# Performance work log

Hardware: AMD Instinct MI355X
Metric: run time of the kernel (lower is better)

Reference implementation:

```python
import jax, jax.numpy as jnp
import numpy as np

J6, J3 = 13, 30          # joints with 6-dim and 3-dim outputs (contiguous groups)
J = J6 + J3              # 43 joints total
D = 512                  # latent_dim
B, T = 16, 196


def setup_inputs() -> dict:
    key = jax.random.key(0)
    ks = jax.random.split(key, 7)
    s = 0.02  # weight init scale
    return {
        "x":   jax.random.normal(ks[0], (B, T, J, D), dtype=jnp.float32),
        "W1":  jax.random.normal(ks[1], (J, D, D), dtype=jnp.float32) * s,
        "b1":  jax.random.normal(ks[2], (J, D), dtype=jnp.float32) * s,
        "W2a": jax.random.normal(ks[3], (J6, D, 6), dtype=jnp.float32) * s,
        "b2a": jax.random.normal(ks[4], (J6, 6), dtype=jnp.float32) * s,
        "W2b": jax.random.normal(ks[5], (J3, D, 3), dtype=jnp.float32) * s,
        "b2b": jax.random.normal(ks[6], (J3, 3), dtype=jnp.float32) * s,
    }


def reference(x, W1, b1, W2a, b2a, W2b, b2b):
    # Per-joint MLP: Linear(D,D) -> GELU -> Linear(D,out_dim_j), concatenated
    # over joints along the last dim (heterogeneous 'dk' mode, vectorized).
    h = jnp.einsum('btjd,jde->btje', x, W1) + b1          # [B,T,J,D]
    h = jax.nn.gelu(h, approximate=False)                  # torch nn.GELU (erf)
    oa = jnp.einsum('btjd,jdo->btjo', h[:, :, :J6], W2a) + b2a  # [B,T,13,6]
    ob = jnp.einsum('btjd,jdo->btjo', h[:, :, J6:], W2b) + b2b  # [B,T,30,3]
    b, t = x.shape[0], x.shape[1]
    # torch.cat(out_list, dim=-1) in joint order == group-wise reshape + concat
    motion = jnp.concatenate([oa.reshape(b, t, -1), ob.reshape(b, t, -1)], axis=-1)
    return motion  # [B, T, 13*6 + 30*3] = [B, T, 168]
```

## Files before the change

### kernel.cpp

```cpp
#include <hip/hip_runtime.h>
#include <hip/hip_bf16.h>

typedef unsigned short ushort_t;
typedef short short8 __attribute__((ext_vector_type(8)));
typedef float f32x4 __attribute__((ext_vector_type(4)));

#define J_TOT 43
#define J6 13
#define D_DIM 512
#define BT 3136
#define OUTW 168

__device__ __forceinline__ unsigned short bf16rne(float f) {
    unsigned u = __builtin_bit_cast(unsigned, f);
    u += 0x7fffu + ((u >> 16) & 1u);
    return (unsigned short)(u >> 16);
}

__device__ __forceinline__ float gelu_f(float v) {
    float t = v * __builtin_fmaf(v * v, 0.0356774081f, 0.7978845608f);
    float e = __builtin_amdgcn_exp2f(t * 2.8853900818f);
    float s = __builtin_amdgcn_rcpf(1.0f + e);
    return __builtin_fmaf(-v, s, v);
}

__device__ __forceinline__ void async_ld16(const void* gsrc, void* ldst) {
    __builtin_amdgcn_global_load_lds(
        (const __attribute__((address_space(1))) unsigned int*)(unsigned long long)(const char*)gsrc,
        (__attribute__((address_space(3))) unsigned int*)ldst,
        16, 0, 0);
}

__global__ void w1_transpose_kernel(const float* __restrict__ W1, ushort_t* __restrict__ W1t) {
    __shared__ ushort_t tile[64][74];
    const int j = blockIdx.z;
    const int t = threadIdx.x;
    const int d0 = blockIdx.x * 64, e0 = blockIdx.y * 64;
    const float* src = W1 + (size_t)j * D_DIM * D_DIM;
    const int el = t & 63, dl = t >> 6;
#pragma unroll
    for (int i = 0; i < 16; i++) {
        int d = dl + i * 4;
        tile[el][d] = bf16rne(src[(size_t)(d0 + d) * D_DIM + e0 + el]);
    }
    __syncthreads();
    ushort_t* dst = W1t + (size_t)j * D_DIM * D_DIM;
#pragma unroll
    for (int i = 0; i < 16; i++) {
        int n = dl + i * 4;
        dst[(size_t)(e0 + n) * D_DIM + d0 + el] = tile[n][el];
    }
}

__global__ void w2_pack_kernel(const float* __restrict__ W2a, const float* __restrict__ b2a,
                               const float* __restrict__ W2b, const float* __restrict__ b2b,
                               ushort_t* __restrict__ W2t, float* __restrict__ b2p) {
    const int j = blockIdx.x;
    const int t = threadIdx.x;
    const int odim = (j < J6) ? 6 : 3;
    const float* w = (j < J6) ? (W2a + (size_t)j * D_DIM * 6) : (W2b + (size_t)(j - J6) * D_DIM * 3);
    for (int idx = t; idx < 16 * D_DIM; idx += 256) {
        int o = idx >> 9, k = idx & 511;
        float v = (o < odim) ? w[(size_t)k * odim + o] : 0.0f;
        W2t[(size_t)j * 16 * D_DIM + idx] = bf16rne(v);
    }
    if (t < 16) {
        const float* bb = (j < J6) ? (b2a + (size_t)j * 6) : (b2b + (size_t)(j - J6) * 3);
        b2p[j * 16 + t] = (t < odim) ? bb[t] : 0.0f;
    }
}

__global__ __launch_bounds__(256, 2)
void MotionDecoder_36309653520632_kernel(const float* __restrict__ x,
                                         const float* __restrict__ b1,
                                         const ushort_t* __restrict__ W1t,
                                         const ushort_t* __restrict__ W2t,
                                         const float* __restrict__ b2p,
                                         float* __restrict__ out) {
    __shared__ unsigned char smem[32768];
    char* as_base = (char*)smem;
    char* bs_base = (char*)smem + 16384;
    char* hs_base = (char*)smem;

    const int j   = blockIdx.y;
    const int m0  = blockIdx.x * 128;
    const int tid = threadIdx.x;
    const int lane = tid & 63;
    const int wid  = tid >> 6;
    const int wrow = (wid >> 1) * 64;
    const int wcol = (wid & 1) * 64;

    const int a_m  = tid >> 1;
    const int a_k0 = (tid & 1) * 32;
    int a_row = m0 + a_m; if (a_row > BT - 1) a_row = BT - 1;
    const float* xrow = x + ((size_t)a_row * J_TOT + j) * D_DIM;

    const ushort_t* w1j = W1t + (size_t)j * D_DIM * D_DIM;
    const ushort_t* w2j = W2t + (size_t)j * 16 * D_DIM;

    f32x4 acc2[4];
#pragma unroll
    for (int r = 0; r < 4; r++) acc2[r] = (f32x4){0.f, 0.f, 0.f, 0.f};

    for (int nt = 0; nt < 4; nt++) {
        const int n0 = nt * 128;
        f32x4 acc[4][4];
#pragma unroll
        for (int a = 0; a < 4; a++)
#pragma unroll
            for (int b = 0; b < 4; b++) acc[a][b] = (f32x4){0.f, 0.f, 0.f, 0.f};

        for (int ks = 0; ks < 8; ks++) {
#pragma unroll
            for (int pass = 0; pass < 4; pass++) {
                int n = pass * 32 + wid * 8 + (lane >> 3);
                int cg = (lane & 7) ^ (n & 7);
                const ushort_t* gsrc = w1j + (size_t)(n0 + n) * D_DIM + ks * 64 + cg * 8;
                char* ldst = bs_base + (pass * 32 + wid * 8) * 128;
                async_ld16(gsrc, ldst);
            }
            const float* ap = xrow + ks * 64 + a_k0;
            float4 f[8];
#pragma unroll
            for (int i = 0; i < 8; i++) f[i] = ((const float4*)ap)[i];
#pragma unroll
            for (int c = 0; c < 4; c++) {
                union { unsigned short s[8]; uint4 v; } pk;
                float4 u0 = f[2 * c], u1 = f[2 * c + 1];
                pk.s[0] = bf16rne(u0.x); pk.s[1] = bf16rne(u0.y);
                pk.s[2] = bf16rne(u0.z); pk.s[3] = bf16rne(u0.w);
                pk.s[4] = bf16rne(u1.x); pk.s[5] = bf16rne(u1.y);
                pk.s[6] = bf16rne(u1.z); pk.s[7] = bf16rne(u1.w);
                int ch = (a_k0 >> 3) + c;
                int sw = ch ^ (a_m & 7);
                *(uint4*)(as_base + a_m * 128 + sw * 16) = pk.v;
            }
            __syncthreads();
#pragma unroll
            for (int kk = 0; kk < 2; kk++) {
                short8 af[4], bfr[4];
                int chv = kk * 4 + (lane >> 4);
#pragma unroll
                for (int rt = 0; rt < 4; rt++) {
                    int m = wrow + rt * 16 + (lane & 15);
                    af[rt] = *(const short8*)(as_base + m * 128 + ((chv ^ (m & 7)) * 16));
                }
#pragma unroll
                for (int ct = 0; ct < 4; ct++) {
                    int n = wcol + ct * 16 + (lane & 15);
                    bfr[ct] = *(const short8*)(bs_base + n * 128 + ((chv ^ (n & 7)) * 16));
                }
#pragma unroll
                for (int rt = 0; rt < 4; rt++)
#pragma unroll
                    for (int ct = 0; ct < 4; ct++)
                        acc[rt][ct] = __builtin_amdgcn_mfma_f32_16x16x32_bf16(
                            af[rt], bfr[ct], acc[rt][ct], 0, 0, 0);
            }
            __syncthreads();
        }

#pragma unroll
        for (int ct = 0; ct < 4; ct++) {
            int ncol = wcol + ct * 16 + (lane & 15);
            float bv = b1[j * D_DIM + n0 + ncol];
            int c2 = ncol >> 3;
            int boff = (ncol & 7) * 2;
#pragma unroll
            for (int rt = 0; rt < 4; rt++) {
                int mb = wrow + rt * 16 + ((lane >> 4) << 2);
#pragma unroll
                for (int r = 0; r < 4; r++) {
                    float g = gelu_f(acc[rt][ct][r] + bv);
                    int m = mb + r;
                    int sw = c2 ^ (m & 15);
                    *(unsigned short*)(hs_base + m * 256 + sw * 16 + boff) = bf16rne(g);
                }
            }
        }
        __syncthreads();

        if (wid < 2) {
            short8 wf[4];
#pragma unroll
            for (int kk2 = 0; kk2 < 4; kk2++) {
                const ushort_t* gsrc = w2j + (size_t)(lane & 15) * D_DIM + n0 + kk2 * 32 + (lane >> 4) * 8;
                wf[kk2] = *(const short8*)gsrc;
            }
#pragma unroll
            for (int rt = 0; rt < 4; rt++) {
                int m = wid * 64 + rt * 16 + (lane & 15);
#pragma unroll
                for (int kk2 = 0; kk2 < 4; kk2++) {
                    int ch = kk2 * 4 + (lane >> 4);
                    short8 a2 = *(const short8*)(hs_base + m * 256 + ((ch ^ (m & 15)) * 16));
                    acc2[rt] = __builtin_amdgcn_mfma_f32_16x16x32_bf16(a2, wf[kk2], acc2[rt], 0, 0, 0);
                }
            }
        }
        __syncthreads();
    }

    if (wid < 2) {
        int o = lane & 15;
        int odim = (j < J6) ? 6 : 3;
        int cb = (j < J6) ? j * 6 : 78 + (j - J6) * 3;
        float bo = b2p[j * 16 + o];
        if (o < odim) {
#pragma unroll
            for (int rt = 0; rt < 4; rt++) {
#pragma unroll
                for (int r = 0; r < 4; r++) {
                    int m = m0 + wid * 64 + rt * 16 + ((lane >> 4) << 2) + r;
                    if (m < BT) out[(size_t)m * OUTW + cb + o] = acc2[rt][r] + bo;
                }
            }
        }
    }
}

extern "C" void kernel_launch(void* const* d_in, const int* in_sizes, int n_in,
                              void* d_out, int out_size, void* d_ws, size_t ws_size,
                              hipStream_t stream) {
    const float* x   = (const float*)d_in[0];
    const float* W1  = (const float*)d_in[1];
    const float* b1  = (const float*)d_in[2];
    const float* W2a = (const float*)d_in[3];
    const float* b2a = (const float*)d_in[4];
    const float* W2b = (const float*)d_in[5];
    const float* b2b = (const float*)d_in[6];
    float* out = (float*)d_out;

    ushort_t* W1t = (ushort_t*)d_ws;
    ushort_t* W2t = W1t + (size_t)J_TOT * D_DIM * D_DIM;
    float*    b2p = (float*)(W2t + (size_t)J_TOT * 16 * D_DIM);

    w1_transpose_kernel<<<dim3(8, 8, J_TOT), 256, 0, stream>>>(W1, W1t);
    w2_pack_kernel<<<J_TOT, 256, 0, stream>>>(W2a, b2a, W2b, b2b, W2t, b2p);
    MotionDecoder_36309653520632_kernel<<<dim3(25, J_TOT), 256, 0, stream>>>(
        x, b1, W1t, W2t, b2p, out);
}
```

Before: 654.2 us.

## Pre-convert x to bf16 and stream A tiles via async LDS loads

Adds a separate pass that converts all of x to bf16 in workspace. When the workspace is large enough, the main kernel then loads A tiles with global_load_lds exactly as it loads W1, instead of doing fp32 register loads, per-tile conversion and LDS stores. It also precomputes the per-pass source and destination pointers and raises the launch-bounds occupancy hint from 2 to 4. The cost is an extra full read of x (about 276 MB) plus a bf16 write and re-read, and the whole path depends on the workspace being big enough.

```diff
diff --git a/kernel.cpp b/kernel.cpp
--- a/kernel.cpp
+++ b/kernel.cpp
@@ -29,6 +29,18 @@
         (const __attribute__((address_space(1))) unsigned int*)(unsigned long long)(const char*)gsrc,
         (__attribute__((address_space(3))) unsigned int*)ldst,
         16, 0, 0);
+}
+
+__global__ void x_convert_kernel(const float* __restrict__ x, ushort_t* __restrict__ xb) {
+    size_t i = ((size_t)blockIdx.x * 256 + threadIdx.x) * 8;
+    float4 f0 = *(const float4*)(x + i);
+    float4 f1 = *(const float4*)(x + i + 4);
+    union { unsigned short s[8]; uint4 v; } pk;
+    pk.s[0] = bf16rne(f0.x); pk.s[1] = bf16rne(f0.y);
+    pk.s[2] = bf16rne(f0.z); pk.s[3] = bf16rne(f0.w);
+    pk.s[4] = bf16rne(f1.x); pk.s[5] = bf16rne(f1.y);
+    pk.s[6] = bf16rne(f1.z); pk.s[7] = bf16rne(f1.w);
+    *(uint4*)(xb + i) = pk.v;
 }
 
 __global__ void w1_transpose_kernel(const float* __restrict__ W1, ushort_t* __restrict__ W1t) {
@@ -70,13 +82,15 @@
     }
 }
 
-__global__ __launch_bounds__(256, 2)
-void MotionDecoder_36309653520632_kernel(const float* __restrict__ x,
-                                         const float* __restrict__ b1,
-                                         const ushort_t* __restrict__ W1t,
-                                         const ushort_t* __restrict__ W2t,
-                                         const float* __restrict__ b2p,
-                                         float* __restrict__ out) {
+template <bool XB>
+__global__ __launch_bounds__(256, 4)
+void md_main(const float* __restrict__ x,
+             const ushort_t* __restrict__ xbf,
+             const float* __restrict__ b1,
+             const ushort_t* __restrict__ W1t,
+             const ushort_t* __restrict__ W2t,
+             const float* __restrict__ b2p,
+             float* __restrict__ out) {
     __shared__ unsigned char smem[32768];
     char* as_base = (char*)smem;
     char* bs_base = (char*)smem + 16384;
@@ -90,13 +104,29 @@
     const int wrow = (wid >> 1) * 64;
     const int wcol = (wid & 1) * 64;
 
+    const ushort_t* w1j = W1t + (size_t)j * D_DIM * D_DIM;
+    const ushort_t* w2j = W2t + (size_t)j * 16 * D_DIM;
+
+    const int sg   = lane >> 3;
+    const int cg   = (lane & 7) ^ (sg & 7);
+    const ushort_t* a_src[4];
+    const ushort_t* b_src[4];
+    char* a_dst[4];
+    char* b_dst[4];
+#pragma unroll
+    for (int pass = 0; pass < 4; pass++) {
+        int rr = pass * 32 + wid * 8 + sg;
+        int arow = m0 + rr; if (arow > BT - 1) arow = BT - 1;
+        a_src[pass] = xbf + ((size_t)arow * J_TOT + j) * D_DIM + cg * 8;
+        b_src[pass] = w1j + (size_t)rr * D_DIM + cg * 8;
+        a_dst[pass] = as_base + (pass * 32 + wid * 8) * 128;
+        b_dst[pass] = bs_base + (pass * 32 + wid * 8) * 128;
+    }
+
     const int a_m  = tid >> 1;
     const int a_k0 = (tid & 1) * 32;
     int a_row = m0 + a_m; if (a_row > BT - 1) a_row = BT - 1;
-    const float* xrow = x + ((size_t)a_row * J_TOT + j) * D_DIM;
-
-    const ushort_t* w1j = W1t + (size_t)j * D_DIM * D_DIM;
-    const ushort_t* w2j = W2t + (size_t)j * 16 * D_DIM;
+    const float* xrow = XB ? nullptr : (x + ((size_t)a_row * J_TOT + j) * D_DIM);
 
     f32x4 acc2[4];
 #pragma unroll
@@ -111,29 +141,32 @@
             for (int b = 0; b < 4; b++) acc[a][b] = (f32x4){0.f, 0.f, 0.f, 0.f};
 
         for (int ks = 0; ks < 8; ks++) {
-#pragma unroll
-            for (int pass = 0; pass < 4; pass++) {
-                int n = pass * 32 + wid * 8 + (lane >> 3);
-                int cg = (lane & 7) ^ (n & 7);
-                const ushort_t* gsrc = w1j + (size_t)(n0 + n) * D_DIM + ks * 64 + cg * 8;
-                char* ldst = bs_base + (pass * 32 + wid * 8) * 128;
-                async_ld16(gsrc, ldst);
-            }
-            const float* ap = xrow + ks * 64 + a_k0;
-            float4 f[8];
-#pragma unroll
-            for (int i = 0; i < 8; i++) f[i] = ((const float4*)ap)[i];
-#pragma unroll
-            for (int c = 0; c < 4; c++) {
-                union { unsigned short s[8]; uint4 v; } pk;
-                float4 u0 = f[2 * c], u1 = f[2 * c + 1];
-                pk.s[0] = bf16rne(u0.x); pk.s[1] = bf16rne(u0.y);
-                pk.s[2] = bf16rne(u0.z); pk.s[3] = bf16rne(u0.w);
-                pk.s[4] = bf16rne(u1.x); pk.s[5] = bf16rne(u1.y);
-                pk.s[6] = bf16rne(u1.z); pk.s[7] = bf16rne(u1.w);
-                int ch = (a_k0 >> 3) + c;
-                int sw = ch ^ (a_m & 7);
-                *(uint4*)(as_base + a_m * 128 + sw * 16) = pk.v;
+            const size_t boff = (size_t)n0 * D_DIM + ks * 64;
+            const size_t aoff = (size_t)ks * 64;
+#pragma unroll
+            for (int pass = 0; pass < 4; pass++)
+                async_ld16(b_src[pass] + boff, b_dst[pass]);
+            if (XB) {
+#pragma unroll
+                for (int pass = 0; pass < 4; pass++)
+                    async_ld16(a_src[pass] + aoff, a_dst[pass]);
+            } else {
+                const float* ap = xrow + ks * 64 + a_k0;
+                float4 f[8];
+#pragma unroll
+                for (int i = 0; i < 8; i++) f[i] = ((const float4*)ap)[i];
+#pragma unroll
+                for (int c = 0; c < 4; c++) {
+                    union { unsigned short s[8]; uint4 v; } pk;
+                    float4 u0 = f[2 * c], u1 = f[2 * c + 1];
+                    pk.s[0] = bf16rne(u0.x); pk.s[1] = bf16rne(u0.y);
+                    pk.s[2] = bf16rne(u0.z); pk.s[3] = bf16rne(u0.w);
+                    pk.s[4] = bf16rne(u1.x); pk.s[5] = bf16rne(u1.y);
+                    pk.s[6] = bf16rne(u1.z); pk.s[7] = bf16rne(u1.w);
+                    int ch = (a_k0 >> 3) + c;
+                    int sw = ch ^ (a_m & 7);
+                    *(uint4*)(as_base + a_m * 128 + sw * 16) = pk.v;
+                }
             }
             __syncthreads();
 #pragma unroll
@@ -165,7 +198,7 @@
             int ncol = wcol + ct * 16 + (lane & 15);
             float bv = b1[j * D_DIM + n0 + ncol];
             int c2 = ncol >> 3;
-            int boff = (ncol & 7) * 2;
+            int boff2 = (ncol & 7) * 2;
 #pragma unroll
             for (int rt = 0; rt < 4; rt++) {
                 int mb = wrow + rt * 16 + ((lane >> 4) << 2);
@@ -174,7 +207,7 @@
                     float g = gelu_f(acc[rt][ct][r] + bv);
                     int m = mb + r;
                     int sw = c2 ^ (m & 15);
-                    *(unsigned short*)(hs_base + m * 256 + sw * 16 + boff) = bf16rne(g);
+                    *(unsigned short*)(hs_base + m * 256 + sw * 16 + boff2) = bf16rne(g);
                 }
             }
         }
@@ -234,9 +267,16 @@
     ushort_t* W1t = (ushort_t*)d_ws;
     ushort_t* W2t = W1t + (size_t)J_TOT * D_DIM * D_DIM;
     float*    b2p = (float*)(W2t + (size_t)J_TOT * 16 * D_DIM);
+    ushort_t* xbf = (ushort_t*)((char*)d_ws + 23251648);
+    const size_t ws_needed = 23251648ull + 138084352ull;
 
     w1_transpose_kernel<<<dim3(8, 8, J_TOT), 256, 0, stream>>>(W1, W1t);
     w2_pack_kernel<<<J_TOT, 256, 0, stream>>>(W2a, b2a, W2b, b2b, W2t, b2p);
-    MotionDecoder_36309653520632_kernel<<<dim3(25, J_TOT), 256, 0, stream>>>(
-        x, b1, W1t, W2t, b2p, out);
-}
+
+    if (ws_size >= ws_needed) {
+        x_convert_kernel<<<33712, 256, 0, stream>>>(x, xbf);
+        md_main<true><<<dim3(25, J_TOT), 256, 0, stream>>>(x, xbf, b1, W1t, W2t, b2p, out);
+    } else {
+        md_main<false><<<dim3(25, J_TOT), 256, 0, stream>>>(x, xbf, b1, W1t, W2t, b2p, out);
+    }
+}
```

Result: slower. 768.0 us (+17.4%).

## Keep full bf16 activation row tile resident in LDS and double-buffer W1

Applied to the files above, without the earlier changes.

Loads and converts the 128x512 activation tile for a joint once into a 128 KB LDS buffer, instead of re-reading and converting x for each of the four output column tiles. W1 tiles are now prefetched into registers two steps ahead and written into alternating LDS buffers, replacing the single-buffer async global-to-LDS loads. This cuts global traffic on x several-fold but uses 160 KB of LDS, which drops occupancy to one block per CU and leaves less latency hiding.

```diff
diff --git a/kernel.cpp b/kernel.cpp
--- a/kernel.cpp
+++ b/kernel.cpp
@@ -22,13 +22,6 @@
     float e = __builtin_amdgcn_exp2f(t * 2.8853900818f);
     float s = __builtin_amdgcn_rcpf(1.0f + e);
     return __builtin_fmaf(-v, s, v);
-}
-
-__device__ __forceinline__ void async_ld16(const void* gsrc, void* ldst) {
-    __builtin_amdgcn_global_load_lds(
-        (const __attribute__((address_space(1))) unsigned int*)(unsigned long long)(const char*)gsrc,
-        (__attribute__((address_space(3))) unsigned int*)ldst,
-        16, 0, 0);
 }
 
 __global__ void w1_transpose_kernel(const float* __restrict__ W1, ushort_t* __restrict__ W1t) {
@@ -70,17 +63,18 @@
     }
 }
 
-__global__ __launch_bounds__(256, 2)
-void MotionDecoder_36309653520632_kernel(const float* __restrict__ x,
-                                         const float* __restrict__ b1,
-                                         const ushort_t* __restrict__ W1t,
-                                         const ushort_t* __restrict__ W2t,
-                                         const float* __restrict__ b2p,
-                                         float* __restrict__ out) {
-    __shared__ unsigned char smem[32768];
-    char* as_base = (char*)smem;
-    char* bs_base = (char*)smem + 16384;
-    char* hs_base = (char*)smem;
+__global__ __launch_bounds__(256, 1)
+void md_main(const float* __restrict__ x,
+             const float* __restrict__ b1,
+             const ushort_t* __restrict__ W1t,
+             const ushort_t* __restrict__ W2t,
+             const float* __restrict__ b2p,
+             float* __restrict__ out) {
+    __shared__ unsigned char smem[163840];
+    char* const As = (char*)smem;
+    char* const B0 = (char*)smem + 131072;
+    char* const B1 = (char*)smem + 147456;
+    char* const Hs = (char*)smem + 131072;
 
     const int j   = blockIdx.y;
     const int m0  = blockIdx.x * 128;
@@ -89,66 +83,95 @@
     const int wid  = tid >> 6;
     const int wrow = (wid >> 1) * 64;
     const int wcol = (wid & 1) * 64;
-
-    const int a_m  = tid >> 1;
-    const int a_k0 = (tid & 1) * 32;
-    int a_row = m0 + a_m; if (a_row > BT - 1) a_row = BT - 1;
-    const float* xrow = x + ((size_t)a_row * J_TOT + j) * D_DIM;
+    const int quad = lane >> 4;
+    const int l16  = lane & 15;
 
     const ushort_t* w1j = W1t + (size_t)j * D_DIM * D_DIM;
     const ushort_t* w2j = W2t + (size_t)j * 16 * D_DIM;
 
-    f32x4 acc2[4];
-#pragma unroll
-    for (int r = 0; r < 4; r++) acc2[r] = (f32x4){0.f, 0.f, 0.f, 0.f};
-
-    for (int nt = 0; nt < 4; nt++) {
-        const int n0 = nt * 128;
-        f32x4 acc[4][4];
-#pragma unroll
-        for (int a = 0; a < 4; a++)
-#pragma unroll
-            for (int b = 0; b < 4; b++) acc[a][b] = (f32x4){0.f, 0.f, 0.f, 0.f};
-
-        for (int ks = 0; ks < 8; ks++) {
-#pragma unroll
-            for (int pass = 0; pass < 4; pass++) {
-                int n = pass * 32 + wid * 8 + (lane >> 3);
-                int cg = (lane & 7) ^ (n & 7);
-                const ushort_t* gsrc = w1j + (size_t)(n0 + n) * D_DIM + ks * 64 + cg * 8;
-                char* ldst = bs_base + (pass * 32 + wid * 8) * 128;
-                async_ld16(gsrc, ldst);
-            }
-            const float* ap = xrow + ks * 64 + a_k0;
+    const int bn  = tid >> 1;
+    const int bc0 = (tid & 1) * 4;
+    const ushort_t* bsrc = w1j + (size_t)bn * D_DIM + bc0 * 8;
+    int bws[4];
+#pragma unroll
+    for (int c = 0; c < 4; c++) bws[c] = bn * 128 + (((bc0 + c) ^ (bn & 7)) * 16);
+
+    uint4 pa[4], pb[4];
+#define ISSUE_B(g, p)                                                             \
+    {                                                                             \
+        const ushort_t* s_ = bsrc + (size_t)((g) >> 3) * 128 * D_DIM + ((g) & 7) * 64; \
+        p[0] = *(const uint4*)(s_);      p[1] = *(const uint4*)(s_ + 8);          \
+        p[2] = *(const uint4*)(s_ + 16); p[3] = *(const uint4*)(s_ + 24);         \
+    }
+#define WRITE_B(dst, p)                                                           \
+    {                                                                             \
+        *(uint4*)((dst) + bws[0]) = p[0]; *(uint4*)((dst) + bws[1]) = p[1];       \
+        *(uint4*)((dst) + bws[2]) = p[2]; *(uint4*)((dst) + bws[3]) = p[3];       \
+    }
+
+    ISSUE_B(0, pa);
+    ISSUE_B(1, pb);
+
+    {
+        const int ar = tid >> 1;
+        const int ap = tid & 1;
+        int arow = m0 + ar; if (arow > BT - 1) arow = BT - 1;
+        const float4* xr4 = (const float4*)(x + ((size_t)arow * J_TOT + j) * D_DIM + ap * 256);
+        char* arow_base = As + ar * 1024;
+        const int asw = ar & 63;
+#pragma unroll
+        for (int b = 0; b < 8; b++) {
             float4 f[8];
 #pragma unroll
-            for (int i = 0; i < 8; i++) f[i] = ((const float4*)ap)[i];
-#pragma unroll
-            for (int c = 0; c < 4; c++) {
+            for (int i = 0; i < 8; i++) f[i] = xr4[b * 8 + i];
+#pragma unroll
+            for (int i = 0; i < 4; i++) {
                 union { unsigned short s[8]; uint4 v; } pk;
-                float4 u0 = f[2 * c], u1 = f[2 * c + 1];
+                float4 u0 = f[2 * i], u1 = f[2 * i + 1];
                 pk.s[0] = bf16rne(u0.x); pk.s[1] = bf16rne(u0.y);
                 pk.s[2] = bf16rne(u0.z); pk.s[3] = bf16rne(u0.w);
                 pk.s[4] = bf16rne(u1.x); pk.s[5] = bf16rne(u1.y);
                 pk.s[6] = bf16rne(u1.z); pk.s[7] = bf16rne(u1.w);
-                int ch = (a_k0 >> 3) + c;
-                int sw = ch ^ (a_m & 7);
-                *(uint4*)(as_base + a_m * 128 + sw * 16) = pk.v;
-            }
-            __syncthreads();
+                int ch = ap * 32 + b * 4 + i;
+                *(uint4*)(arow_base + ((ch ^ asw) * 16)) = pk.v;
+            }
+        }
+    }
+
+    f32x4 acc2[4];
+#pragma unroll
+    for (int r = 0; r < 4; r++) acc2[r] = (f32x4){0.f, 0.f, 0.f, 0.f};
+
+    for (int nt = 0; nt < 4; nt++) {
+        const int n0 = nt * 128;
+        f32x4 acc[4][4];
+#pragma unroll
+        for (int a = 0; a < 4; a++)
+#pragma unroll
+            for (int b = 0; b < 4; b++) acc[a][b] = (f32x4){0.f, 0.f, 0.f, 0.f};
+
+        WRITE_B(B0, pa);
+#pragma unroll
+        for (int c = 0; c < 4; c++) pa[c] = pb[c];
+        ISSUE_B(nt * 8 + 2, pb);
+        __syncthreads();
+
+        for (int ks = 0; ks < 8; ks++) {
+            char* const bcur = (ks & 1) ? B1 : B0;
 #pragma unroll
             for (int kk = 0; kk < 2; kk++) {
                 short8 af[4], bfr[4];
-                int chv = kk * 4 + (lane >> 4);
+                const int cha = ks * 8 + kk * 4 + quad;
+                const int chb = kk * 4 + quad;
 #pragma unroll
                 for (int rt = 0; rt < 4; rt++) {
-                    int m = wrow + rt * 16 + (lane & 15);
-                    af[rt] = *(const short8*)(as_base + m * 128 + ((chv ^ (m & 7)) * 16));
+                    int m = wrow + rt * 16 + l16;
+                    af[rt] = *(const short8*)(As + m * 1024 + ((cha ^ (m & 63)) * 16));
                 }
 #pragma unroll
                 for (int ct = 0; ct < 4; ct++) {
-                    int n = wcol + ct * 16 + (lane & 15);
-                    bfr[ct] = *(const short8*)(bs_base + n * 128 + ((chv ^ (n & 7)) * 16));
+                    int n = wcol + ct * 16 + l16;
+                    bfr[ct] = *(const short8*)(bcur + n * 128 + ((chb ^ (n & 7)) * 16));
                 }
 #pragma unroll
                 for (int rt = 0; rt < 4; rt++)
@@ -157,24 +180,30 @@
                         acc[rt][ct] = __builtin_amdgcn_mfma_f32_16x16x32_bf16(
                             af[rt], bfr[ct], acc[rt][ct], 0, 0, 0);
             }
+            if (ks < 7) {
+                WRITE_B(((ks + 1) & 1) ? B1 : B0, pa);
+#pragma unroll
+                for (int c = 0; c < 4; c++) pa[c] = pb[c];
+                int g = nt * 8 + ks + 3;
+                if (g < 32) ISSUE_B(g, pb);
+            }
             __syncthreads();
         }
 
 #pragma unroll
         for (int ct = 0; ct < 4; ct++) {
-            int ncol = wcol + ct * 16 + (lane & 15);
+            int ncol = wcol + ct * 16 + l16;
             float bv = b1[j * D_DIM + n0 + ncol];
             int c2 = ncol >> 3;
-            int boff = (ncol & 7) * 2;
+            int boff2 = (ncol & 7) * 2;
 #pragma unroll
             for (int rt = 0; rt < 4; rt++) {
-                int mb = wrow + rt * 16 + ((lane >> 4) << 2);
+                int mb = wrow + rt * 16 + quad * 4;
 #pragma unroll
                 for (int r = 0; r < 4; r++) {
                     float g = gelu_f(acc[rt][ct][r] + bv);
                     int m = mb + r;
-                    int sw = c2 ^ (m & 15);
-                    *(unsigned short*)(hs_base + m * 256 + sw * 16 + boff) = bf16rne(g);
+                    *(unsigned short*)(Hs + m * 256 + ((c2 ^ (m & 15)) * 16) + boff2) = bf16rne(g);
                 }
             }
         }
@@ -184,16 +213,16 @@
             short8 wf[4];
 #pragma unroll
             for (int kk2 = 0; kk2 < 4; kk2++) {
-                const ushort_t* gsrc = w2j + (size_t)(lane & 15) * D_DIM + n0 + kk2 * 32 + (lane >> 4) * 8;
+                const ushort_t* gsrc = w2j + (size_t)l16 * D_DIM + n0 + kk2 * 32 + quad * 8;
                 wf[kk2] = *(const short8*)gsrc;
             }
 #pragma unroll
             for (int rt = 0; rt < 4; rt++) {
-                int m = wid * 64 + rt * 16 + (lane & 15);
+                int m = wid * 64 + rt * 16 + l16;
 #pragma unroll
                 for (int kk2 = 0; kk2 < 4; kk2++) {
-                    int ch = kk2 * 4 + (lane >> 4);
-                    short8 a2 = *(const short8*)(hs_base + m * 256 + ((ch ^ (m & 15)) * 16));
+                    int ch = kk2 * 4 + quad;
+                    short8 a2 = *(const short8*)(Hs + m * 256 + ((ch ^ (m & 15)) * 16));
                     acc2[rt] = __builtin_amdgcn_mfma_f32_16x16x32_bf16(a2, wf[kk2], acc2[rt], 0, 0, 0);
                 }
             }
@@ -202,7 +231,7 @@
     }
 
     if (wid < 2) {
-        int o = lane & 15;
+        int o = l16;
         int odim = (j < J6) ? 6 : 3;
         int cb = (j < J6) ? j * 6 : 78 + (j - J6) * 3;
         float bo = b2p[j * 16 + o];
@@ -211,12 +240,14 @@
             for (int rt = 0; rt < 4; rt++) {
 #pragma unroll
                 for (int r = 0; r < 4; r++) {
-                    int m = m0 + wid * 64 + rt * 16 + ((lane >> 4) << 2) + r;
+                    int m = m0 + wid * 64 + rt * 16 + quad * 4 + r;
                     if (m < BT) out[(size_t)m * OUTW + cb + o] = acc2[rt][r] + bo;
                 }
             }
         }
     }
+#undef ISSUE_B
+#undef WRITE_B
 }
 
 extern "C" void kernel_launch(void* const* d_in, const int* in_sizes, int n_in,
@@ -237,6 +268,5 @@
 
     w1_transpose_kernel<<<dim3(8, 8, J_TOT), 256, 0, stream>>>(W1, W1t);
     w2_pack_kernel<<<J_TOT, 256, 0, stream>>>(W2a, b2a, W2b, b2b, W2t, b2p);
-    MotionDecoder_36309653520632_kernel<<<dim3(25, J_TOT), 256, 0, stream>>>(
-        x, b1, W1t, W2t, b2p, out);
-}
+    md_main<<<dim3(25, J_TOT), 256, 0, stream>>>(x, b1, W1t, W2t, b2p, out);
+}
```

After: 835.1 us. +27.6%, slower.

## Pre-convert x to bf16 and register-prefetch GEMM tiles one step ahead

Applied to the files above, without the earlier changes.

Adds a separate kernel that converts x to bf16 once, so the main kernel loads half as many bytes for A and no longer converts inside the k-loop, which was redone for each of the four N tiles. The main loop now prefetches the next A and B tiles into registers while the MFMAs run, then stores them to LDS, in place of async global-to-LDS loads. Launch bounds are raised to 3 blocks per SM and one trailing barrier is removed. In exchange, the extra conversion pass costs a full read and write of x, and the register pressure goes up.

```diff
diff --git a/kernel.cpp b/kernel.cpp
--- a/kernel.cpp
+++ b/kernel.cpp
@@ -24,11 +24,16 @@
     return __builtin_fmaf(-v, s, v);
 }
 
-__device__ __forceinline__ void async_ld16(const void* gsrc, void* ldst) {
-    __builtin_amdgcn_global_load_lds(
-        (const __attribute__((address_space(1))) unsigned int*)(unsigned long long)(const char*)gsrc,
-        (__attribute__((address_space(3))) unsigned int*)ldst,
-        16, 0, 0);
+__global__ void x_convert_kernel(const float* __restrict__ x, ushort_t* __restrict__ xb) {
+    size_t i = ((size_t)blockIdx.x * 256 + threadIdx.x) * 8;
+    float4 f0 = *(const float4*)(x + i);
+    float4 f1 = *(const float4*)(x + i + 4);
+    union { unsigned short s[8]; uint4 v; } pk;
+    pk.s[0] = bf16rne(f0.x); pk.s[1] = bf16rne(f0.y);
+    pk.s[2] = bf16rne(f0.z); pk.s[3] = bf16rne(f0.w);
+    pk.s[4] = bf16rne(f1.x); pk.s[5] = bf16rne(f1.y);
+    pk.s[6] = bf16rne(f1.z); pk.s[7] = bf16rne(f1.w);
+    *(uint4*)(xb + i) = pk.v;
 }
 
 __global__ void w1_transpose_kernel(const float* __restrict__ W1, ushort_t* __restrict__ W1t) {
@@ -70,17 +75,17 @@
     }
 }
 
-__global__ __launch_bounds__(256, 2)
-void MotionDecoder_36309653520632_kernel(const float* __restrict__ x,
-                                         const float* __restrict__ b1,
-                                         const ushort_t* __restrict__ W1t,
-                                         const ushort_t* __restrict__ W2t,
-                                         const float* __restrict__ b2p,
-                                         float* __restrict__ out) {
+__global__ __launch_bounds__(256, 3)
+void md_main(const ushort_t* __restrict__ xbf,
+             const float* __restrict__ b1,
+             const ushort_t* __restrict__ W1t,
+             const ushort_t* __restrict__ W2t,
+             const float* __restrict__ b2p,
+             float* __restrict__ out) {
     __shared__ unsigned char smem[32768];
-    char* as_base = (char*)smem;
-    char* bs_base = (char*)smem + 16384;
-    char* hs_base = (char*)smem;
+    char* const as_base = (char*)smem;
+    char* const bs_base = (char*)smem + 16384;
+    char* const hs_base = (char*)smem;
 
     const int j   = blockIdx.y;
     const int m0  = blockIdx.x * 128;
@@ -89,14 +94,38 @@
     const int wid  = tid >> 6;
     const int wrow = (wid >> 1) * 64;
     const int wcol = (wid & 1) * 64;
-
-    const int a_m  = tid >> 1;
-    const int a_k0 = (tid & 1) * 32;
-    int a_row = m0 + a_m; if (a_row > BT - 1) a_row = BT - 1;
-    const float* xrow = x + ((size_t)a_row * J_TOT + j) * D_DIM;
+    const int quad = lane >> 4;
+    const int l16  = lane & 15;
 
     const ushort_t* w1j = W1t + (size_t)j * D_DIM * D_DIM;
     const ushort_t* w2j = W2t + (size_t)j * 16 * D_DIM;
+
+    const int r_st = tid >> 1;
+    const int hp   = tid & 1;
+    int gr = m0 + r_st; if (gr > BT - 1) gr = BT - 1;
+    const ushort_t* a_g = xbf + ((size_t)gr * J_TOT + j) * D_DIM + hp * 32;
+    const ushort_t* b_g = w1j + (size_t)r_st * D_DIM + hp * 32;
+    int wds[4];
+#pragma unroll
+    for (int c = 0; c < 4; c++)
+        wds[c] = r_st * 128 + (((hp * 4 + c) ^ (r_st & 7)) * 16);
+
+    uint4 pA[4], pB[4];
+#define ISSUE_A(ks)                                                       \
+    {                                                                     \
+        const ushort_t* s_ = a_g + (ks) * 64;                             \
+        pA[0] = *(const uint4*)(s_);      pA[1] = *(const uint4*)(s_ + 8);\
+        pA[2] = *(const uint4*)(s_ + 16); pA[3] = *(const uint4*)(s_ + 24);\
+    }
+#define ISSUE_B(nt, ks)                                                   \
+    {                                                                     \
+        const ushort_t* s_ = b_g + (size_t)(nt) * 128 * D_DIM + (ks) * 64;\
+        pB[0] = *(const uint4*)(s_);      pB[1] = *(const uint4*)(s_ + 8);\
+        pB[2] = *(const uint4*)(s_ + 16); pB[3] = *(const uint4*)(s_ + 24);\
+    }
+
+    ISSUE_A(0);
+    ISSUE_B(0, 0);
 
     f32x4 acc2[4];
 #pragma unroll
@@ -111,43 +140,31 @@
             for (int b = 0; b < 4; b++) acc[a][b] = (f32x4){0.f, 0.f, 0.f, 0.f};
 
         for (int ks = 0; ks < 8; ks++) {
-#pragma unroll
-            for (int pass = 0; pass < 4; pass++) {
-                int n = pass * 32 + wid * 8 + (lane >> 3);
-                int cg = (lane & 7) ^ (n & 7);
-                const ushort_t* gsrc = w1j + (size_t)(n0 + n) * D_DIM + ks * 64 + cg * 8;
-                char* ldst = bs_base + (pass * 32 + wid * 8) * 128;
-                async_ld16(gsrc, ldst);
-            }
-            const float* ap = xrow + ks * 64 + a_k0;
-            float4 f[8];
-#pragma unroll
-            for (int i = 0; i < 8; i++) f[i] = ((const float4*)ap)[i];
-#pragma unroll
-            for (int c = 0; c < 4; c++) {
-                union { unsigned short s[8]; uint4 v; } pk;
-                float4 u0 = f[2 * c], u1 = f[2 * c + 1];
-                pk.s[0] = bf16rne(u0.x); pk.s[1] = bf16rne(u0.y);
-                pk.s[2] = bf16rne(u0.z); pk.s[3] = bf16rne(u0.w);
-                pk.s[4] = bf16rne(u1.x); pk.s[5] = bf16rne(u1.y);
-                pk.s[6] = bf16rne(u1.z); pk.s[7] = bf16rne(u1.w);
-                int ch = (a_k0 >> 3) + c;
-                int sw = ch ^ (a_m & 7);
-                *(uint4*)(as_base + a_m * 128 + sw * 16) = pk.v;
-            }
             __syncthreads();
+#pragma unroll
+            for (int c = 0; c < 4; c++) *(uint4*)(as_base + wds[c]) = pA[c];
+#pragma unroll
+            for (int c = 0; c < 4; c++) *(uint4*)(bs_base + wds[c]) = pB[c];
+            __syncthreads();
+
+            {
+                int nks = ks + 1, nnt = nt;
+                if (nks == 8) { nks = 0; nnt++; }
+                if (nnt < 4) { ISSUE_A(nks); ISSUE_B(nnt, nks); }
+            }
+
 #pragma unroll
             for (int kk = 0; kk < 2; kk++) {
                 short8 af[4], bfr[4];
-                int chv = kk * 4 + (lane >> 4);
+                const int chv = kk * 4 + quad;
 #pragma unroll
                 for (int rt = 0; rt < 4; rt++) {
-                    int m = wrow + rt * 16 + (lane & 15);
+                    int m = wrow + rt * 16 + l16;
                     af[rt] = *(const short8*)(as_base + m * 128 + ((chv ^ (m & 7)) * 16));
                 }
 #pragma unroll
                 for (int ct = 0; ct < 4; ct++) {
-                    int n = wcol + ct * 16 + (lane & 15);
+                    int n = wcol + ct * 16 + l16;
                     bfr[ct] = *(const short8*)(bs_base + n * 128 + ((chv ^ (n & 7)) * 16));
                 }
 #pragma unroll
@@ -157,24 +174,24 @@
                         acc[rt][ct] = __builtin_amdgcn_mfma_f32_16x16x32_bf16(
                             af[rt], bfr[ct], acc[rt][ct], 0, 0, 0);
             }
-            __syncthreads();
-        }
+        }
+
+        __syncthreads();
 
 #pragma unroll
         for (int ct = 0; ct < 4; ct++) {
-            int ncol = wcol + ct * 16 + (lane & 15);
+            int ncol = wcol + ct * 16 + l16;
             float bv = b1[j * D_DIM + n0 + ncol];
             int c2 = ncol >> 3;
-            int boff = (ncol & 7) * 2;
+            int boff2 = (ncol & 7) * 2;
 #pragma unroll
             for (int rt = 0; rt < 4; rt++) {
-                int mb = wrow + rt * 16 + ((lane >> 4) << 2);
+                int mb = wrow + rt * 16 + quad * 4;
 #pragma unroll
                 for (int r = 0; r < 4; r++) {
                     float g = gelu_f(acc[rt][ct][r] + bv);
                     int m = mb + r;
-                    int sw = c2 ^ (m & 15);
-                    *(unsigned short*)(hs_base + m * 256 + sw * 16 + boff) = bf16rne(g);
+                    *(unsigned short*)(hs_base + m * 256 + ((c2 ^ (m & 15)) * 16) + boff2) = bf16rne(g);
                 }
             }
         }
@@ -184,25 +201,24 @@
             short8 wf[4];
 #pragma unroll
             for (int kk2 = 0; kk2 < 4; kk2++) {
-                const ushort_t* gsrc = w2j + (size_t)(lane & 15) * D_DIM + n0 + kk2 * 32 + (lane >> 4) * 8;
+                const ushort_t* gsrc = w2j + (size_t)l16 * D_DIM + n0 + kk2 * 32 + quad * 8;
                 wf[kk2] = *(const short8*)gsrc;
             }
 #pragma unroll
             for (int rt = 0; rt < 4; rt++) {
-                int m = wid * 64 + rt * 16 + (lane & 15);
+                int m = wid * 64 + rt * 16 + l16;
 #pragma unroll
                 for (int kk2 = 0; kk2 < 4; kk2++) {
-                    int ch = kk2 * 4 + (lane >> 4);
+                    int ch = kk2 * 4 + quad;
                     short8 a2 = *(const short8*)(hs_base + m * 256 + ((ch ^ (m & 15)) * 16));
                     acc2[rt] = __builtin_amdgcn_mfma_f32_16x16x32_bf16(a2, wf[kk2], acc2[rt], 0, 0, 0);
                 }
             }
         }
-        __syncthreads();
     }
 
     if (wid < 2) {
-        int o = lane & 15;
+        int o = l16;
         int odim = (j < J6) ? 6 : 3;
         int cb = (j < J6) ? j * 6 : 78 + (j - J6) * 3;
         float bo = b2p[j * 16 + o];
@@ -211,12 +227,14 @@
             for (int rt = 0; rt < 4; rt++) {
 #pragma unroll
                 for (int r = 0; r < 4; r++) {
-                    int m = m0 + wid * 64 + rt * 16 + ((lane >> 4) << 2) + r;
+                    int m = m0 + wid * 64 + rt * 16 + quad * 4 + r;
                     if (m < BT) out[(size_t)m * OUTW + cb + o] = acc2[rt][r] + bo;
                 }
             }
         }
     }
+#undef ISSUE_A
+#undef ISSUE_B
 }
 
 extern "C" void kernel_launch(void* const* d_in, const int* in_sizes, int n_in,
@@ -234,9 +252,10 @@
     ushort_t* W1t = (ushort_t*)d_ws;
     ushort_t* W2t = W1t + (size_t)J_TOT * D_DIM * D_DIM;
     float*    b2p = (float*)(W2t + (size_t)J_TOT * 16 * D_DIM);
+    ushort_t* xbf = (ushort_t*)((char*)d_ws + 23251648);
 
     w1_transpose_kernel<<<dim3(8, 8, J_TOT), 256, 0, stream>>>(W1, W1t);
     w2_pack_kernel<<<J_TOT, 256, 0, stream>>>(W2a, b2a, W2b, b2b, W2t, b2p);
-    MotionDecoder_36309653520632_kernel<<<dim3(25, J_TOT), 256, 0, stream>>>(
-        x, b1, W1t, W2t, b2p, out);
-}
+    x_convert_kernel<<<33712, 256, 0, stream>>>(x, xbf);
+    md_main<<<dim3(25, J_TOT), 256, 0, stream>>>(xbf, b1, W1t, W2t, b2p, out);
+}
```

Result: slower. 1.099 ms (+68.0%).
